# Kernel tuning notes

Measured on AMD Instinct MI355X. Metric: run time of the kernel, lower is better.

The kernel has to match this reference:

```python
import jax, jax.numpy as jnp
import numpy as np


def setup_inputs() -> dict:
    key = jax.random.key(0)
    k1, k2 = jax.random.split(key)
    B, T, D = 32, 512, 512
    x = jax.random.normal(k1, (B, T, D), dtype=jnp.float32)
    duration = jax.random.randint(k2, (B, T), 0, 8, dtype=jnp.int64)
    return {"x": x, "duration": duration, "max_len": 4096}


def reference(x, duration, max_len):
    # x: [B, T, D]; duration: [B, T] ints; output: [B, max_len, D]
    B, T, D = x.shape
    csum = jnp.cumsum(duration, axis=1)            # [B, T] end offsets per phoneme
    mel_len = csum[:, -1].astype(jnp.int64)        # [B]
    frames = jnp.arange(max_len)                   # [L]
    # frame j belongs to phoneme i where csum[i-1] <= j < csum[i]
    # == searchsorted(csum, j, side='right')
    idx = jax.vmap(lambda c: jnp.searchsorted(c, frames, side='right'))(csum)  # [B, L]
    idx_c = jnp.minimum(idx, T - 1)                # clamp out-of-range (padded region)
    out = jnp.take_along_axis(x, idx_c[..., None], axis=1)  # [B, L, D]
    mask = frames[None, :] < mel_len[:, None]      # [B, L] valid frames
    out = out * mask[..., None].astype(x.dtype)    # zero-pad beyond mel_len
    return out, mel_len
```

## Files before the change

### kernel.cpp

```cpp
#include <hip/hip_runtime.h>
#include <hip/hip_bf16.h>


typedef float f32x4 __attribute__((ext_vector_type(4)));

constexpr int B   = 32;
constexpr int T   = 512;
constexpr int D   = 512;
constexpr int D4  = D / 4;
constexpr int ML  = 4096;
constexpr int NTHREADS = 512;
constexpr int kPhonPerBlock = 8;
constexpr int kNumExp  = T / kPhonPerBlock;
constexpr int kZChunk  = 512;
constexpr int kNumZero = ML / kZChunk;
constexpr int kBlocksPerBatch = kNumExp + kNumZero;

__global__ __launch_bounds__(NTHREADS) void lr_expand(
    const int*   __restrict__ duration,
    const f32x4* __restrict__ x,
    f32x4*       __restrict__ out,
    float*       __restrict__ mel_out)
{
    const int b    = blockIdx.x / kBlocksPerBatch;
    const int r    = blockIdx.x % kBlocksPerBatch;
    const int t    = threadIdx.x;
    const int lane = t & 63;
    const int wave = t >> 6;

    __shared__ int csum[T];
    __shared__ int wsum[NTHREADS / 64];

    int v = duration[b * T + t];
    #pragma unroll
    for (int off = 1; off < 64; off <<= 1) {
        int n = __shfl_up(v, off, 64);
        if (lane >= off) v += n;
    }
    if (lane == 63) wsum[wave] = v;
    __syncthreads();
    int prev = 0;
    #pragma unroll
    for (int w = 0; w < NTHREADS / 64; ++w)
        if (w < wave) prev += wsum[w];
    v += prev;
    csum[t] = v;
    __syncthreads();

    const int mel = csum[T - 1];

    if (r < kNumExp) {
        const int p     = r * kPhonPerBlock + wave;
        const int end   = csum[p];
        const int start = (p == 0) ? 0 : csum[p - 1];

        if (r == 0 && t == 0)
            mel_out[b] = (float)mel;

        if (end > start) {
            const size_t xbase = ((size_t)(b * T + p)) * D4;
            const f32x4 v0 = x[xbase + lane];
            const f32x4 v1 = x[xbase + 64 + lane];
            size_t o = ((size_t)(b * ML + start)) * D4;
            for (int j = start; j < end; ++j, o += D4) {
                out[o + lane]      = v0;
                out[o + 64 + lane] = v1;
            }
        }
    } else {
        const int c  = r - kNumExp;
        const int j0 = c * kZChunk;
        int fstart = mel - j0;
        if (fstart >= kZChunk) return;
        if (fstart < 0) fstart = 0;
        const int total = (kZChunk - fstart) * D4;
        const size_t base = ((size_t)(b * ML + j0 + fstart)) * D4;
        const f32x4 zero = {0.f, 0.f, 0.f, 0.f};
        for (int m = t; m < total; m += NTHREADS)
            out[base + m] = zero;
    }
}

extern "C" void kernel_launch(void* const* d_in, const int* in_sizes, int n_in,
                              void* d_out, int out_size, void* d_ws, size_t ws_size,
                              hipStream_t stream) {
    const float* x   = (const float*)d_in[0];
    const int*   dur = (const int*)d_in[1];

    float* out     = (float*)d_out;
    float* mel_out = out + (size_t)B * ML * D;

    lr_expand<<<B * kBlocksPerBatch, NTHREADS, 0, stream>>>(
        dur, (const f32x4*)x, (f32x4*)out, mel_out);
}
```

Before: 63.69 us.

## Split prefix-sum into separate kernel and shrink zero-fill chunks

Moves the per-batch duration prefix sum into its own small kernel that writes cumulative offsets to workspace. Before, every block of the expand kernel recomputed the full 512-element scan. The main kernel now reads offsets from global memory instead. Zero-fill chunks shrink from 512 to 64 frames, which gives more, smaller zero blocks for better load balance. The cost is an extra kernel launch and a serial dependency between the two kernels.

After: 58.26 us, median of 2. 8.5% less time.

```diff
diff --git a/kernel.cpp b/kernel.cpp
--- a/kernel.cpp
+++ b/kernel.cpp
@@ -10,25 +10,21 @@
 constexpr int D4  = D / 4;
 constexpr int ML  = 4096;
 constexpr int NTHREADS = 512;
-constexpr int kPhonPerBlock = 8;
-constexpr int kNumExp  = T / kPhonPerBlock;
-constexpr int kZChunk  = 512;
-constexpr int kNumZero = ML / kZChunk;
-constexpr int kBlocksPerBatch = kNumExp + kNumZero;
+constexpr int kZChunk = 64;
+constexpr int kNumZ   = ML / kZChunk;
+constexpr int kNumE   = T / 8;
+constexpr int kBPB    = kNumE + kNumZ;
 
-__global__ __launch_bounds__(NTHREADS) void lr_expand(
-    const int*   __restrict__ duration,
-    const f32x4* __restrict__ x,
-    f32x4*       __restrict__ out,
-    float*       __restrict__ mel_out)
+__global__ __launch_bounds__(NTHREADS) void lr_scan(
+    const int* __restrict__ duration,
+    int*       __restrict__ csum,
+    float*     __restrict__ mel_out)
 {
-    const int b    = blockIdx.x / kBlocksPerBatch;
-    const int r    = blockIdx.x % kBlocksPerBatch;
-    const int t    = threadIdx.x;
+    const int b = blockIdx.x;
+    const int t = threadIdx.x;
     const int lane = t & 63;
     const int wave = t >> 6;
 
-    __shared__ int csum[T];
     __shared__ int wsum[NTHREADS / 64];
 
     int v = duration[b * T + t];
@@ -44,40 +40,50 @@
     for (int w = 0; w < NTHREADS / 64; ++w)
         if (w < wave) prev += wsum[w];
     v += prev;
-    csum[t] = v;
-    __syncthreads();
+    csum[b * T + t] = v;
+    if (t == T - 1)
+        mel_out[b] = (float)v;
+}
 
-    const int mel = csum[T - 1];
+__global__ __launch_bounds__(NTHREADS) void lr_main(
+    const int*   __restrict__ csum,
+    const f32x4* __restrict__ x,
+    f32x4*       __restrict__ out)
+{
+    const int bid  = blockIdx.x;
+    const int b    = bid / kBPB;
+    const int r    = bid % kBPB;
+    const int t    = threadIdx.x;
+    const int lane = t & 63;
+    const int wave = t >> 6;
 
-    if (r < kNumExp) {
-        const int p     = r * kPhonPerBlock + wave;
-        const int end   = csum[p];
-        const int start = (p == 0) ? 0 : csum[p - 1];
-
-        if (r == 0 && t == 0)
-            mel_out[b] = (float)mel;
-
-        if (end > start) {
-            const size_t xbase = ((size_t)(b * T + p)) * D4;
-            const f32x4 v0 = x[xbase + lane];
-            const f32x4 v1 = x[xbase + 64 + lane];
-            size_t o = ((size_t)(b * ML + start)) * D4;
-            for (int j = start; j < end; ++j, o += D4) {
+    if (r < kNumE) {
+        const int p   = r * 8 + wave;
+        const int e   = csum[b * T + p];
+        const int s   = (p == 0) ? 0 : csum[b * T + p - 1];
+        if (e > s) {
+            const size_t xb = ((size_t)(b * T + p)) * D4;
+            const f32x4 v0 = x[xb + lane];
+            const f32x4 v1 = x[xb + 64 + lane];
+            size_t o = ((size_t)(b * ML + s)) * D4;
+            for (int j = s; j < e; ++j, o += D4) {
                 out[o + lane]      = v0;
                 out[o + 64 + lane] = v1;
             }
         }
     } else {
-        const int c  = r - kNumExp;
-        const int j0 = c * kZChunk;
-        int fstart = mel - j0;
-        if (fstart >= kZChunk) return;
-        if (fstart < 0) fstart = 0;
-        const int total = (kZChunk - fstart) * D4;
-        const size_t base = ((size_t)(b * ML + j0 + fstart)) * D4;
-        const f32x4 zero = {0.f, 0.f, 0.f, 0.f};
-        for (int m = t; m < total; m += NTHREADS)
-            out[base + m] = zero;
+        const int c   = r - kNumE;
+        const int mel = csum[b * T + T - 1];
+        const int j0  = c * kZChunk;
+        const int lo  = (j0 > mel) ? j0 : mel;
+        const int hi  = j0 + kZChunk;
+        if (lo < hi) {
+            const f32x4 zero = {0.f, 0.f, 0.f, 0.f};
+            const size_t base = ((size_t)(b * ML + lo)) * D4;
+            const int total = (hi - lo) * D4;
+            for (int m = t; m < total; m += NTHREADS)
+                out[base + m] = zero;
+        }
     }
 }
 
@@ -89,7 +95,8 @@
 
     float* out     = (float*)d_out;
     float* mel_out = out + (size_t)B * ML * D;
+    int*   csum    = (int*)d_ws;
 
-    lr_expand<<<B * kBlocksPerBatch, NTHREADS, 0, stream>>>(
-        dur, (const f32x4*)x, (f32x4*)out, mel_out);
+    lr_scan<<<B, NTHREADS, 0, stream>>>(dur, csum, mel_out);
+    lr_main<<<B * kBPB, NTHREADS, 0, stream>>>(csum, (const f32x4*)x, (f32x4*)out);
 }
```

## Compute prefix sum per wave without LDS and rebalance expand/zero block split

Applied to the files above, without the earlier changes.

Each wave now loads all 512 durations as int4 vectors and computes the inclusive scan in registers with a single wave-level shuffle scan, removing shared memory and both __syncthreads. Expand blocks now handle 64 phonemes each (8 per wave, sequentially), and there are fewer of them. Zero-fill blocks shrink to 64-frame chunks, giving many more, finer-grained blocks. The intent is to cut per-block scan overhead and spread the zero-fill writes more evenly, at the cost of longer serial store loops per wave in the expand blocks.

After: 60.53 us. -5.0%, faster.

```diff
diff --git a/kernel.cpp b/kernel.cpp
--- a/kernel.cpp
+++ b/kernel.cpp
@@ -10,74 +10,82 @@
 constexpr int D4  = D / 4;
 constexpr int ML  = 4096;
 constexpr int NTHREADS = 512;
-constexpr int kPhonPerBlock = 8;
-constexpr int kNumExp  = T / kPhonPerBlock;
-constexpr int kZChunk  = 512;
-constexpr int kNumZero = ML / kZChunk;
-constexpr int kBlocksPerBatch = kNumExp + kNumZero;
+constexpr int kNumE   = 8;
+constexpr int kZChunk = 64;
+constexpr int kNumZ   = ML / kZChunk;
 
-__global__ __launch_bounds__(NTHREADS) void lr_expand(
+__global__ __launch_bounds__(NTHREADS) void lr_all(
     const int*   __restrict__ duration,
     const f32x4* __restrict__ x,
     f32x4*       __restrict__ out,
     float*       __restrict__ mel_out)
 {
-    const int b    = blockIdx.x / kBlocksPerBatch;
-    const int r    = blockIdx.x % kBlocksPerBatch;
+    const int bid  = blockIdx.x;
+    const bool isE = bid < B * kNumE;
+    const int b    = isE ? bid / kNumE : (bid - B * kNumE) / kNumZ;
+    const int r    = isE ? bid % kNumE : (bid - B * kNumE) % kNumZ;
     const int t    = threadIdx.x;
     const int lane = t & 63;
     const int wave = t >> 6;
 
-    __shared__ int csum[T];
-    __shared__ int wsum[NTHREADS / 64];
-
-    int v = duration[b * T + t];
+    const int4* d4p = (const int4*)(duration + b * T);
+    const int4 a = d4p[2 * lane];
+    const int4 c = d4p[2 * lane + 1];
+    int p0 = a.x,      p1 = p0 + a.y, p2 = p1 + a.z, p3 = p2 + a.w;
+    int p4 = p3 + c.x, p5 = p4 + c.y, p6 = p5 + c.z, p7 = p6 + c.w;
+    int s = p7;
     #pragma unroll
     for (int off = 1; off < 64; off <<= 1) {
-        int n = __shfl_up(v, off, 64);
-        if (lane >= off) v += n;
+        int n = __shfl_up(s, off, 64);
+        if (lane >= off) s += n;
     }
-    if (lane == 63) wsum[wave] = v;
-    __syncthreads();
-    int prev = 0;
-    #pragma unroll
-    for (int w = 0; w < NTHREADS / 64; ++w)
-        if (w < wave) prev += wsum[w];
-    v += prev;
-    csum[t] = v;
-    __syncthreads();
+    const int excl = s - p7;
+    p0 += excl; p1 += excl; p2 += excl; p3 += excl;
+    p4 += excl; p5 += excl; p6 += excl; p7 += excl;
 
-    const int mel = csum[T - 1];
+    const int mel = __shfl(p7, 63, 64);
 
-    if (r < kNumExp) {
-        const int p     = r * kPhonPerBlock + wave;
-        const int end   = csum[p];
-        const int start = (p == 0) ? 0 : csum[p - 1];
+    if (isE) {
+        const int Lsrc = 8 * r + wave;
+        int e[8];
+        e[0] = __shfl(p0, Lsrc, 64); e[1] = __shfl(p1, Lsrc, 64);
+        e[2] = __shfl(p2, Lsrc, 64); e[3] = __shfl(p3, Lsrc, 64);
+        e[4] = __shfl(p4, Lsrc, 64); e[5] = __shfl(p5, Lsrc, 64);
+        e[6] = __shfl(p6, Lsrc, 64); e[7] = __shfl(p7, Lsrc, 64);
+        const int sprev = __shfl(p7, (Lsrc == 0) ? 0 : Lsrc - 1, 64);
+        int start0 = (Lsrc == 0) ? 0 : sprev;
 
         if (r == 0 && t == 0)
             mel_out[b] = (float)mel;
 
-        if (end > start) {
-            const size_t xbase = ((size_t)(b * T + p)) * D4;
-            const f32x4 v0 = x[xbase + lane];
-            const f32x4 v1 = x[xbase + 64 + lane];
-            size_t o = ((size_t)(b * ML + start)) * D4;
-            for (int j = start; j < end; ++j, o += D4) {
-                out[o + lane]      = v0;
-                out[o + 64 + lane] = v1;
+        const int pbase = 64 * r + 8 * wave;
+        int st = start0;
+        #pragma unroll
+        for (int k = 0; k < 8; ++k) {
+            const int en = e[k];
+            if (en > st) {
+                const size_t xb = ((size_t)(b * T + pbase + k)) * D4;
+                const f32x4 v0 = x[xb + lane];
+                const f32x4 v1 = x[xb + 64 + lane];
+                size_t o = ((size_t)(b * ML + st)) * D4;
+                for (int j = st; j < en; ++j, o += D4) {
+                    out[o + lane]      = v0;
+                    out[o + 64 + lane] = v1;
+                }
             }
+            st = en;
         }
     } else {
-        const int c  = r - kNumExp;
-        const int j0 = c * kZChunk;
-        int fstart = mel - j0;
-        if (fstart >= kZChunk) return;
-        if (fstart < 0) fstart = 0;
-        const int total = (kZChunk - fstart) * D4;
-        const size_t base = ((size_t)(b * ML + j0 + fstart)) * D4;
-        const f32x4 zero = {0.f, 0.f, 0.f, 0.f};
-        for (int m = t; m < total; m += NTHREADS)
-            out[base + m] = zero;
+        const int j0 = r * kZChunk;
+        const int lo = (j0 > mel) ? j0 : mel;
+        const int hi = j0 + kZChunk;
+        if (lo < hi) {
+            const f32x4 zero = {0.f, 0.f, 0.f, 0.f};
+            const size_t base = ((size_t)(b * ML + lo)) * D4;
+            const int total = (hi - lo) * D4;
+            for (int m = t; m < total; m += NTHREADS)
+                out[base + m] = zero;
+        }
     }
 }
 
@@ -90,6 +98,6 @@
     float* out     = (float*)d_out;
     float* mel_out = out + (size_t)B * ML * D;
 
-    lr_expand<<<B * kBlocksPerBatch, NTHREADS, 0, stream>>>(
+    lr_all<<<B * (kNumE + kNumZ), NTHREADS, 0, stream>>>(
         dur, (const f32x4*)x, (f32x4*)out, mel_out);
 }
```
